# Performance work log

Hardware: AMD Instinct MI355X
Metric: run time of the kernel (lower is better)

Reference implementation:

```python
import jax, jax.numpy as jnp
import numpy as np


def setup_inputs() -> dict:
    key = jax.random.key(0)
    k1, k2, k3 = jax.random.split(key, 3)
    B, S, A, C = 128, 52, 5, 20
    predictions = jax.random.normal(k1, (B, A * (5 + C), S, S), dtype=jnp.float32)
    t = jax.random.uniform(k2, (B, S, S, A, 5 + C), dtype=jnp.float32)
    mask = (jax.random.uniform(k3, (B, S, S, A)) < 0.05).astype(jnp.float32)
    targets = t.at[..., 4].set(mask)
    anchors = jnp.array([[1.08, 1.19], [3.42, 4.41], [6.63, 11.38],
                         [9.42, 5.11], [16.62, 10.52]], dtype=jnp.float32)
    return {"predictions": predictions, "targets": targets, "anchors": anchors}


def _yolov2_loss(predictions, targets, anchors):
    B, pred_dim, S, _ = predictions.shape
    A = anchors.shape[0]
    C = pred_dim // A - 5
    # [B, A, 5+C, S, S] -> [B, S, S, A, 5+C]
    p = predictions.reshape(B, A, 5 + C, S, S).transpose(0, 3, 4, 1, 2)
    tx, ty, tw, th = p[..., 0], p[..., 1], p[..., 2], p[..., 3]
    conf_logits = p[..., 4]
    class_logits = p[..., 5:]

    gx, gy, gw, gh = targets[..., 0], targets[..., 1], targets[..., 2], targets[..., 3]
    obj_mask = targets[..., 4]
    class_target = targets[..., 5:]

    pred_cx = jax.nn.sigmoid(tx)
    pred_cy = jax.nn.sigmoid(ty)
    pred_w = jnp.exp(tw) * anchors[:, 0]  # broadcast over trailing A dim
    pred_h = jnp.exp(th) * anchors[:, 1]

    # grid offsets: dim 1 is i (row -> cy), dim 2 is j (col -> cx)
    jj = jnp.arange(S, dtype=jnp.float32)[None, None, :, None]
    ii = jnp.arange(S, dtype=jnp.float32)[None, :, None, None]
    cx_gt, cy_gt = gx + jj, gy + ii
    cx_pr, cy_pr = pred_cx + jj, pred_cy + ii

    # vectorized corner-form IoU (only used where obj_mask == 1)
    x1min, x1max = cx_gt - gw / 2, cx_gt + gw / 2
    y1min, y1max = cy_gt - gh / 2, cy_gt + gh / 2
    x2min, x2max = cx_pr - pred_w / 2, cx_pr + pred_w / 2
    y2min, y2max = cy_pr - pred_h / 2, cy_pr + pred_h / 2
    inter_w = jnp.clip(jnp.minimum(x1max, x2max) - jnp.maximum(x1min, x2min), 0.0)
    inter_h = jnp.clip(jnp.minimum(y1max, y2max) - jnp.maximum(y1min, y2min), 0.0)
    inter = inter_w * inter_h
    union = gw * gh + pred_w * pred_h - inter
    iou = jnp.where(union > 0, inter / union, 0.0)

    loss_xy = jnp.sum(obj_mask * (jnp.square(pred_cx - gx) + jnp.square(pred_cy - gy)))
    eps = 1e-6
    loss_wh = jnp.sum(obj_mask * (jnp.square(jnp.sqrt(pred_w + eps) - jnp.sqrt(gw + eps))
                                  + jnp.square(jnp.sqrt(pred_h + eps) - jnp.sqrt(gh + eps))))

    conf_pred = jax.nn.sigmoid(conf_logits)
    loss_obj = jnp.sum(obj_mask * jnp.square(iou - conf_pred))
    loss_noobj = jnp.sum((1.0 - obj_mask) * jnp.square(conf_pred))

    # BCE with logits: softplus(x) - x * t (stable via logaddexp)
    bce = jnp.logaddexp(0.0, class_logits) - class_logits * class_target
    loss_cls = jnp.sum(obj_mask[..., None] * bce)

    total = 5.0 * (loss_xy + loss_wh) + 5.0 * loss_obj + 0.5 * loss_noobj + loss_cls
    return total, loss_xy + loss_wh, loss_cls, loss_obj + loss_noobj


def reference(predictions, targets, anchors):
    # returns (total, coord, class, obj) matching the original dict values
    return _yolov2_loss(predictions, targets, anchors)
```

## Files before the change

### kernel.cpp

```cpp
#include <hip/hip_runtime.h>

#define SS 2704
#define NA 5
#define NC 20
#define NB 128
#define CELLS (NB * SS)
#define TILE 64
#define TPB 320
#define NBLK (CELLS / TILE)
#define RBLOCK 1024

__device__ __forceinline__ float fast_sigmoid(float x) {
    return __builtin_amdgcn_rcpf(1.0f + __expf(-x));
}
__device__ __forceinline__ float fast_softplus(float x) {
    return fmaxf(x, 0.0f) + __logf(1.0f + __expf(-fabsf(x)));
}

__global__ __launch_bounds__(TPB) void yolo_main(
        const float* __restrict__ P,
        const float* __restrict__ T,
        const float* __restrict__ anch,
        float* __restrict__ partial) {
    __shared__ float red[NA][4];

    int a    = threadIdx.x >> 6;
    int lane = threadIdx.x & 63;
    int cell = blockIdx.x * TILE + lane;
    int b    = cell / SS;
    int ij   = cell - b * SS;

    const float* Ta = T + (size_t)cell * 125 + a * 25;
    const float* Pa = P + ((size_t)b * 125 + a * 25) * SS + ij;
    float aw  = anch[2 * a];
    float ahv = anch[2 * a + 1];

    float fl = Ta[4];
    float cp = fast_sigmoid(Pa[4 * SS]);

    float s_xywh = 0.0f, s_cls = 0.0f, s_obj = 0.0f, s_noobj = 0.0f;

    if (fl != 0.0f) {
        float tx = Pa[0], ty = Pa[SS], tw = Pa[2 * SS], th = Pa[3 * SS];
        float gx = Ta[0], gy = Ta[1], gw = Ta[2], gh = Ta[3];
        float cx = fast_sigmoid(tx), cy = fast_sigmoid(ty);
        float pw = __expf(tw) * aw;
        float ph = __expf(th) * ahv;
        float iw = fmaxf(fminf(gx + 0.5f * gw, cx + 0.5f * pw) -
                         fmaxf(gx - 0.5f * gw, cx - 0.5f * pw), 0.0f);
        float ih = fmaxf(fminf(gy + 0.5f * gh, cy + 0.5f * ph) -
                         fmaxf(gy - 0.5f * gh, cy - 0.5f * ph), 0.0f);
        float inter = iw * ih;
        float uni   = gw * gh + pw * ph - inter;
        float iou   = (uni > 0.0f) ? inter * __builtin_amdgcn_rcpf(uni) : 0.0f;

        float dx = cx - gx, dy = cy - gy;
        s_xywh += dx * dx + dy * dy;
        const float eps = 1e-6f;
        float dw = __fsqrt_rn(pw + eps) - __fsqrt_rn(gw + eps);
        float dh = __fsqrt_rn(ph + eps) - __fsqrt_rn(gh + eps);
        s_xywh += dw * dw + dh * dh;

        float dob = iou - cp;
        s_obj += dob * dob;

        #pragma unroll
        for (int c = 0; c < NC; ++c) {
            float l = Pa[(size_t)(5 + c) * SS];
            float t = Ta[5 + c];
            s_cls += fast_softplus(l) - l * t;
        }
    } else {
        s_noobj = cp * cp;
    }

    #pragma unroll
    for (int off = 32; off > 0; off >>= 1) {
        s_xywh  += __shfl_xor(s_xywh,  off, 64);
        s_cls   += __shfl_xor(s_cls,   off, 64);
        s_obj   += __shfl_xor(s_obj,   off, 64);
        s_noobj += __shfl_xor(s_noobj, off, 64);
    }
    if (lane == 0) {
        red[a][0] = s_xywh; red[a][1] = s_cls; red[a][2] = s_obj; red[a][3] = s_noobj;
    }
    __syncthreads();
    if (threadIdx.x == 0) {
        float r0 = 0, r1 = 0, r2 = 0, r3 = 0;
        #pragma unroll
        for (int w = 0; w < NA; ++w) {
            r0 += red[w][0]; r1 += red[w][1]; r2 += red[w][2]; r3 += red[w][3];
        }
        float* p = partial + (size_t)blockIdx.x * 4;
        p[0] = r0; p[1] = r1; p[2] = r2; p[3] = r3;
    }
}

__global__ __launch_bounds__(RBLOCK) void yolo_reduce(
        const float* __restrict__ partial, int n, float* __restrict__ out) {
    float v0 = 0.0f, v1 = 0.0f, v2 = 0.0f, v3 = 0.0f;
    for (int i = threadIdx.x; i < n; i += RBLOCK) {
        const float* p = partial + (size_t)i * 4;
        v0 += p[0]; v1 += p[1]; v2 += p[2]; v3 += p[3];
    }
    #pragma unroll
    for (int off = 32; off > 0; off >>= 1) {
        v0 += __shfl_xor(v0, off, 64);
        v1 += __shfl_xor(v1, off, 64);
        v2 += __shfl_xor(v2, off, 64);
        v3 += __shfl_xor(v3, off, 64);
    }
    __shared__ float red[RBLOCK / 64][4];
    int wid = threadIdx.x >> 6, lane = threadIdx.x & 63;
    if (lane == 0) {
        red[wid][0] = v0; red[wid][1] = v1; red[wid][2] = v2; red[wid][3] = v3;
    }
    __syncthreads();
    if (threadIdx.x == 0) {
        float xywh = 0, cls = 0, obj = 0, noobj = 0;
        #pragma unroll
        for (int q = 0; q < RBLOCK / 64; ++q) {
            xywh += red[q][0]; cls += red[q][1]; obj += red[q][2]; noobj += red[q][3];
        }
        out[0] = 5.0f * xywh + 5.0f * obj + 0.5f * noobj + cls;
        out[1] = xywh;
        out[2] = cls;
        out[3] = obj + noobj;
    }
}

extern "C" void kernel_launch(void* const* d_in, const int* in_sizes, int n_in,
                              void* d_out, int out_size, void* d_ws, size_t ws_size,
                              hipStream_t stream) {
    const float* P = (const float*)d_in[0];
    const float* T = (const float*)d_in[1];
    const float* anch = (const float*)d_in[2];
    float* out = (float*)d_out;
    float* partial = (float*)d_ws;

    yolo_main<<<NBLK, TPB, 0, stream>>>(P, T, anch, partial);
    yolo_reduce<<<1, RBLOCK, 0, stream>>>(partial, NBLK, out);
}
```

Before: 59.33 us.

## Compact active cells across wave lanes for class-loss computation

```diff
diff --git a/kernel.cpp b/kernel.cpp
--- a/kernel.cpp
+++ b/kernel.cpp
@@ -26,9 +26,12 @@
 
     int a    = threadIdx.x >> 6;
     int lane = threadIdx.x & 63;
-    int cell = blockIdx.x * TILE + lane;
+    int base_cell = blockIdx.x * TILE;
+    int cell = base_cell + lane;
     int b    = cell / SS;
     int ij   = cell - b * SS;
+    int b0   = base_cell / SS;
+    int ij0  = base_cell - b0 * SS;
 
     const float* Ta = T + (size_t)cell * 125 + a * 25;
     const float* Pa = P + ((size_t)b * 125 + a * 25) * SS + ij;
@@ -39,8 +42,9 @@
     float cp = fast_sigmoid(Pa[4 * SS]);
 
     float s_xywh = 0.0f, s_cls = 0.0f, s_obj = 0.0f, s_noobj = 0.0f;
+    bool isobj = (fl != 0.0f);
 
-    if (fl != 0.0f) {
+    if (isobj) {
         float tx = Pa[0], ty = Pa[SS], tw = Pa[2 * SS], th = Pa[3 * SS];
         float gx = Ta[0], gy = Ta[1], gw = Ta[2], gh = Ta[3];
         float cx = fast_sigmoid(tx), cy = fast_sigmoid(ty);
@@ -63,15 +67,35 @@
 
         float dob = iou - cp;
         s_obj += dob * dob;
+    } else {
+        s_noobj = cp * cp;
+    }
 
-        #pragma unroll
-        for (int c = 0; c < NC; ++c) {
-            float l = Pa[(size_t)(5 + c) * SS];
-            float t = Ta[5 + c];
+    unsigned long long act = __ballot(isobj);
+    int nact = __popcll(act);
+    int slot_off = lane / 20;
+    int c = lane - slot_off * 20;
+    unsigned long long m = act;
+    for (int basep = 0; basep < nact; basep += 3) {
+        unsigned long long m0 = m;
+        unsigned long long m1 = m0 & (m0 - 1);
+        unsigned long long m2 = m1 & (m1 - 1);
+        int src0 = __ffsll(m0) - 1;
+        int src1 = __ffsll(m1) - 1;
+        int src2 = __ffsll(m2) - 1;
+        m = m2 & (m2 - 1);
+
+        int s   = basep + slot_off;
+        int src = (slot_off == 0) ? src0 : (slot_off == 1) ? src1 : src2;
+        if (slot_off < 3 && s < nact) {
+            int pij = ij0 + src;
+            int pb  = b0;
+            if (pij >= SS) { pij -= SS; pb += 1; }
+            int pcell = base_cell + src;
+            float t = T[(size_t)pcell * 125 + a * 25 + 5 + c];
+            float l = P[((size_t)pb * 125 + a * 25 + 5 + c) * SS + pij];
             s_cls += fast_softplus(l) - l * t;
         }
-    } else {
-        s_noobj = cp * cp;
     }
 
     #pragma unroll
```

New measurement: 57.38 us. -3.3%, faster.
